# Performance work log

Hardware: AMD Instinct MI355X
Metric: run time of the kernel (lower is better)

## Reference

```python
import jax, jax.numpy as jnp
import numpy as np

N = 8192      # num_nodes
B = 16        # batch
IN_DIM = 2    # input_dim
HID = 64      # hid_dim
K = 2         # diffusion_steps
DEG = 16
E = N * DEG
F = IN_DIM + HID            # concat(input, state) feature dim
NUM_MAT = 2 * K + 1         # dual random walk: 2 matrices * K steps + identity


def _spmm(vals, rows, cols, x):
    # sparse [N,N] @ dense [N,M]: y[rows[e]] += vals[e] * x[cols[e]]
    return jax.ops.segment_sum(vals[:, None] * x[cols], rows, num_segments=N)


def _diff_conv(x, W, b, edge_src, edge_dst, vals1, vals2):
    # x: [B, N, F] -> [B, N*out_dim]; Chebyshev-like diffusion recursion
    x0 = jnp.transpose(x, (1, 2, 0)).reshape(N, F * B)  # [N, F*B]
    xs = [x0]
    # matrix 1 = D_out^-1 A (edges src->dst), matrix 2 = D_in^-1 A^T (edges dst->src)
    for rows, cols, vals in ((edge_src, edge_dst, vals1), (edge_dst, edge_src, vals2)):
        x1 = _spmm(vals, rows, cols, x0)
        xs.append(x1)
        xp, xc = x0, x1
        for _ in range(2, K + 1):
            xn = 2.0 * _spmm(vals, rows, cols, xc) - xp
            xs.append(xn)
            xp, xc = xc, xn
    xstk = jnp.stack(xs, 0).reshape(NUM_MAT, N, F, B)
    xstk = jnp.transpose(xstk, (3, 1, 2, 0)).reshape(B * N, F * NUM_MAT)
    out = xstk @ W + b  # [B*N, out_dim]
    return out.reshape(B, -1)


def setup_inputs() -> dict:
    key = jax.random.key(0)
    k = jax.random.split(key, 8)
    inputs = jax.random.normal(k[0], (B, N * IN_DIM), jnp.float32)
    state = jax.random.normal(k[1], (B, N * HID), jnp.float32)
    edge_src = jax.random.randint(k[2], (E,), 0, N)
    edge_dst = jax.random.randint(k[3], (E,), 0, N)
    a = jax.random.uniform(k[4], (E,), jnp.float32) + 0.1  # positive edge weights
    dout = jax.ops.segment_sum(a, edge_src, num_segments=N)
    din = jax.ops.segment_sum(a, edge_dst, num_segments=N)
    vals1 = a / jnp.where(dout > 0, dout, 1.0)[edge_src]  # random-walk normalize A
    vals2 = a / jnp.where(din > 0, din, 1.0)[edge_dst]    # random-walk normalize A^T
    std_g = 1.414 * np.sqrt(2.0 / (F * NUM_MAT + 2 * HID)).astype(np.float32)
    std_c = 1.414 * np.sqrt(2.0 / (F * NUM_MAT + HID)).astype(np.float32)
    W_gate = jax.random.normal(k[5], (F * NUM_MAT, 2 * HID), jnp.float32) * std_g
    b_gate = jnp.zeros((2 * HID,), jnp.float32)
    W_cand = jax.random.normal(k[6], (F * NUM_MAT, HID), jnp.float32) * std_c
    b_cand = jnp.zeros((HID,), jnp.float32)
    return dict(inputs=inputs, state=state, edge_src=edge_src, edge_dst=edge_dst,
                vals1=vals1, vals2=vals2, W_gate=W_gate, b_gate=b_gate,
                W_cand=W_cand, b_cand=b_cand)


def reference(inputs, state, edge_src, edge_dst, vals1, vals2,
              W_gate, b_gate, W_cand, b_cand):
    i = inputs.reshape(B, N, IN_DIM)
    s = state.reshape(B, N, HID)
    x = jnp.concatenate([i, s], axis=2)  # [B, N, F]
    value = jax.nn.sigmoid(_diff_conv(x, W_gate, b_gate, edge_src, edge_dst, vals1, vals2))
    value = value.reshape(B, N, 2 * HID)
    r = value[..., :HID].reshape(B, N * HID)
    u = value[..., HID:].reshape(B, N * HID)
    rs = (r * state).reshape(B, N, HID)
    xc = jnp.concatenate([i, rs], axis=2)
    c = jnp.tanh(_diff_conv(xc, W_cand, b_cand, edge_src, edge_dst, vals1, vals2))
    new_state = u * state + (1.0 - u) * c
    return (new_state, new_state)
```

## Files before the change

kernel.cpp:

```cpp
#include <hip/hip_runtime.h>
#include <cstddef>
#include <cstdint>

#define NNODES 8192
#define BATCH  16
#define HID    64
#define NEDGE  131072
#define SN     524288
#define OUTHALF 8388608
#define FP2    72
#define SLABU  1152
#define NSTR   5760
#define NSTR4  720
#define XCS4   144
#define KP2    384
#define GN     4

typedef __attribute__((ext_vector_type(8))) short bf16x8;
typedef __attribute__((ext_vector_type(4))) float f32x4;

static __device__ __forceinline__ float bf2f(ushort u) {
    union { uint32_t i; float f; } c; c.i = ((uint32_t)u) << 16; return c.f;
}
static __device__ __forceinline__ ushort f2bf(float f) {
    union { float f; uint32_t i; } c; c.f = f;
    uint32_t lsb = (c.i >> 16) & 1;
    return (ushort)((c.i + 0x7fffu + lsb) >> 16);
}


__global__ void zero_counts_kernel(int* __restrict__ c1, int* __restrict__ c2) {
    int i = blockIdx.x * 256 + threadIdx.x;
    if (i < NNODES) { c1[i] = 0; c2[i] = 0; }
}

__global__ void hist_kernel(const int* __restrict__ src, const int* __restrict__ dst,
                            int* __restrict__ c1, int* __restrict__ c2) {
    int e = blockIdx.x * 256 + threadIdx.x;
    if (e < NEDGE) {
        atomicAdd(&c1[src[e]], 1);
        atomicAdd(&c2[dst[e]], 1);
    }
}

__global__ __launch_bounds__(1024) void scan_kernel(const int* __restrict__ counts,
                                                    int* __restrict__ rowptr,
                                                    int* __restrict__ cursor) {
    __shared__ int sh[1024];
    int tid = threadIdx.x;
    int base = tid * 8;
    int local[8];
    int sum = 0;
#pragma unroll
    for (int j = 0; j < 8; ++j) { local[j] = counts[base + j]; sum += local[j]; }
    sh[tid] = sum;
    __syncthreads();
    for (int off = 1; off < 1024; off <<= 1) {
        int v = (tid >= off) ? sh[tid - off] : 0;
        __syncthreads();
        sh[tid] += v;
        __syncthreads();
    }
    int p = sh[tid] - sum;
#pragma unroll
    for (int j = 0; j < 8; ++j) {
        cursor[base + j] = p;
        p += local[j];
        rowptr[base + j + 1] = p;
    }
    if (tid == 0) rowptr[0] = 0;
}

__global__ void scatter_kernel(const int* __restrict__ src, const int* __restrict__ dst,
                               const float* __restrict__ v1, const float* __restrict__ v2,
                               int* __restrict__ cur1, int* __restrict__ cur2,
                               int* __restrict__ cols1, float* __restrict__ valsC1,
                               int* __restrict__ cols2, float* __restrict__ valsC2) {
    int e = blockIdx.x * 256 + threadIdx.x;
    if (e < NEDGE) {
        int r1 = src[e];
        int p1 = atomicAdd(&cur1[r1], 1);
        cols1[p1] = dst[e];
        valsC1[p1] = v1[e];
        int r2 = dst[e];
        int p2 = atomicAdd(&cur2[r2], 1);
        cols2[p2] = src[e];
        valsC2[p2] = v2[e];
    }
}


__global__ void convert_w_kernel(const float* __restrict__ Wg, const float* __restrict__ Wc,
                                 ushort* __restrict__ WgT, ushort* __restrict__ WcT) {
    int i = blockIdx.x * 256 + threadIdx.x;
    if (i >= 192 * KP2) return;
    int col = i / KP2, k2 = i - col * KP2;
    int m = k2 / FP2, f = k2 - m * FP2;
    bool valid = (m < 5) && (f < 66);
    int ko = f * 5 + m;
    if (col < 128) {
        WgT[col * KP2 + k2] = valid ? f2bf(Wg[ko * 128 + col]) : (ushort)0;
    } else {
        int c = col - 128;
        WcT[c * KP2 + k2] = valid ? f2bf(Wc[ko * 64 + c]) : (ushort)0;
    }
}


__global__ void build_x0_kernel(const float* __restrict__ inputs, const float* __restrict__ state,
                                uint* __restrict__ Xb_u, uint* __restrict__ Xc_u) {
    int t = blockIdx.x * 256 + threadIdx.x;
    if (t >= NNODES * BATCH * 36) return;
    int n = t / 576;
    int r = t - n * 576;
    int b = r / 36;
    int j = r - b * 36;
    int f0 = 2 * j;
    uint val = 0;
    if (f0 == 0) {
        float v0 = inputs[(size_t)b * (NNODES * 2) + n * 2 + 0];
        float v1 = inputs[(size_t)b * (NNODES * 2) + n * 2 + 1];
        val = (uint)f2bf(v0) | ((uint)f2bf(v1) << 16);
    } else if (f0 < 66) {
        float v0 = state[(size_t)b * SN + n * HID + (f0 - 2)];
        float v1 = state[(size_t)b * SN + n * HID + (f0 - 1)];
        val = (uint)f2bf(v0) | ((uint)f2bf(v1) << 16);
    }
    Xb_u[(size_t)n * 2880 + r] = val;
    if (f0 == 0 || f0 >= 66) Xc_u[t] = val;
}


static __device__ __forceinline__ void fma8(float* acc, uint4 d, float v) {
    acc[0] += v * bf2f((ushort)(d.x));  acc[1] += v * bf2f((ushort)(d.x >> 16));
    acc[2] += v * bf2f((ushort)(d.y));  acc[3] += v * bf2f((ushort)(d.y >> 16));
    acc[4] += v * bf2f((ushort)(d.z));  acc[5] += v * bf2f((ushort)(d.z >> 16));
    acc[6] += v * bf2f((ushort)(d.w));  acc[7] += v * bf2f((ushort)(d.w >> 16));
}

static __device__ __forceinline__ uint4 blend_pack8(const float* acc, uint4 p,
                                                    float alpha, float beta) {
    float o[8];
    o[0] = alpha * acc[0] + beta * bf2f((ushort)(p.x));
    o[1] = alpha * acc[1] + beta * bf2f((ushort)(p.x >> 16));
    o[2] = alpha * acc[2] + beta * bf2f((ushort)(p.y));
    o[3] = alpha * acc[3] + beta * bf2f((ushort)(p.y >> 16));
    o[4] = alpha * acc[4] + beta * bf2f((ushort)(p.z));
    o[5] = alpha * acc[5] + beta * bf2f((ushort)(p.z >> 16));
    o[6] = alpha * acc[6] + beta * bf2f((ushort)(p.w));
    o[7] = alpha * acc[7] + beta * bf2f((ushort)(p.w >> 16));
    uint4 r;
    r.x = (uint32_t)f2bf(o[0]) | ((uint32_t)f2bf(o[1]) << 16);
    r.y = (uint32_t)f2bf(o[2]) | ((uint32_t)f2bf(o[3]) << 16);
    r.z = (uint32_t)f2bf(o[4]) | ((uint32_t)f2bf(o[5]) << 16);
    r.w = (uint32_t)f2bf(o[6]) | ((uint32_t)f2bf(o[7]) << 16);
    return r;
}

__global__ __launch_bounds__(64) void spmm_dual8(
        const int* __restrict__ rp1, const int* __restrict__ c1, const float* __restrict__ v1,
        const uint4* __restrict__ x1,
        const int* __restrict__ rp2, const int* __restrict__ c2, const float* __restrict__ v2,
        const uint4* __restrict__ x2,
        int xs,
        const uint4* __restrict__ xp, int ps,
        uint4* __restrict__ y1, uint4* __restrict__ y2, int ys,
        float alpha, float beta) {
    int bid = blockIdx.x;
    int slice = bid & 7;
    int pair  = bid >> 3;
    int n     = pair & 8191;
    int graph = pair >> 13;
    const int* rowptr = graph ? rp2 : rp1;
    const int* cols   = graph ? c2 : c1;
    const float* vals = graph ? v2 : v1;
    const uint4* x    = graph ? x2 : x1;
    uint4* y          = graph ? y2 : y1;

    int t = threadIdx.x;
    int eg = t / 18;
    int li = t - eg * 18;
    int base = slice * 18 + li;
    bool active = t < 54;
    int s = rowptr[n], e = rowptr[n + 1];
    float acc[8] = {0, 0, 0, 0, 0, 0, 0, 0};
    const uint4 uz = make_uint4(0, 0, 0, 0);
    for (int i = s; i < e; i += 6) {
        int iA = i + eg, iB = i + 3 + eg;
        bool okA = active && (iA < e);
        bool okB = active && (iB < e);
        int cA  = okA ? cols[iA] : 0;
        int cB  = okB ? cols[iB] : 0;
        float vA = okA ? vals[iA] : 0.f;
        float vB = okB ? vals[iB] : 0.f;
        uint4 dA = okA ? x[(size_t)cA * xs + base] : uz;
        uint4 dB = okB ? x[(size_t)cB * xs + base] : uz;
        fma8(acc, dA, vA);
        fma8(acc, dB, vB);
    }
#pragma unroll
    for (int j = 0; j < 8; ++j) {
        float a18 = __shfl(acc[j], t + 18);
        float a36 = __shfl(acc[j], t + 36);
        acc[j] += a18 + a36;
    }
    if (t < 18) {
        uint4 p = (beta != 0.f) ? xp[(size_t)n * ps + base] : uz;
        y[(size_t)n * ys + base] = blend_pack8(acc, p, alpha, beta);
    }
}


__global__ __launch_bounds__(256, 2) void gate_mfma(const ushort* __restrict__ Xb,
                                                    const ushort* __restrict__ WgT,
                                                    const float* __restrict__ bg,
                                                    const float* __restrict__ state,
                                                    float* __restrict__ U,
                                                    ushort* __restrict__ Xc) {
    int tid = threadIdx.x;
    int wave = tid >> 6, lane = tid & 63;
    int row = lane & 15, quad = lane >> 4;
    int c0 = wave * 32 + row;
    int c1 = c0 + 16;

    bf16x8 w0[12], w1[12];
#pragma unroll
    for (int kt = 0; kt < 12; ++kt) {
        w0[kt] = *(const bf16x8*)(WgT + (size_t)c0 * KP2 + kt * 32 + quad * 8);
        w1[kt] = *(const bf16x8*)(WgT + (size_t)c1 * KP2 + kt * 32 + quad * 8);
    }
    float bias0 = bg[c0], bias1 = bg[c1];

    int offA[11];
#pragma unroll
    for (int kt = 0; kt < 11; ++kt) {
        int j = 4 * kt + quad;
        int m = j / 9;
        int f0 = 8 * (j - 9 * m);
        offA[kt] = m * SLABU + row * FP2 + f0;
    }
    int off11 = 4 * SLABU + row * FP2 + 64;

    int nodeBase = blockIdx.x * GN;
    for (int g = 0; g < GN; ++g) {
        int n = nodeBase + g;
        const ushort* An = Xb + (size_t)n * NSTR;
        f32x4 acc0 = {0.f, 0.f, 0.f, 0.f};
        f32x4 acc1 = {0.f, 0.f, 0.f, 0.f};
#pragma unroll
        for (int kt = 0; kt < 11; ++kt) {
            bf16x8 av = *(const bf16x8*)(An + offA[kt]);
            acc0 = __builtin_amdgcn_mfma_f32_16x16x32_bf16(av, w0[kt], acc0, 0, 0, 0);
            acc1 = __builtin_amdgcn_mfma_f32_16x16x32_bf16(av, w1[kt], acc1, 0, 0, 0);
        }
        {
            bf16x8 av = {0, 0, 0, 0, 0, 0, 0, 0};
            if (quad == 0) av = *(const bf16x8*)(An + off11);
            acc0 = __builtin_amdgcn_mfma_f32_16x16x32_bf16(av, w0[11], acc0, 0, 0, 0);
            acc1 = __builtin_amdgcn_mfma_f32_16x16x32_bf16(av, w1[11], acc1, 0, 0, 0);
        }
#pragma unroll
        for (int r = 0; r < 4; ++r) {
            int b = quad * 4 + r;
            float v0 = 1.f / (1.f + __expf(-(acc0[r] + bias0)));
            float v1 = 1.f / (1.f + __expf(-(acc1[r] + bias1)));
            if (wave < 2) {
                float s0 = state[(size_t)b * SN + n * HID + c0];
                float s1 = state[(size_t)b * SN + n * HID + c1];
                Xc[(size_t)n * SLABU + b * FP2 + 2 + c0] = f2bf(v0 * s0);
                Xc[(size_t)n * SLABU + b * FP2 + 2 + c1] = f2bf(v1 * s1);
            } else {
                U[(size_t)b * SN + n * HID + (c0 - HID)] = v0;
                U[(size_t)b * SN + n * HID + (c1 - HID)] = v1;
            }
        }
    }
}


__global__ __launch_bounds__(256, 2) void cand_mfma(const ushort* __restrict__ Xb,
                                                    const ushort* __restrict__ Xc,
                                                    const ushort* __restrict__ WcT,
                                                    const float* __restrict__ bc,
                                                    const float* __restrict__ state,
                                                    const float* U,
                                                    float* out) {
    int tid = threadIdx.x;
    int wave = tid >> 6, lane = tid & 63;
    int row = lane & 15, quad = lane >> 4;
    int c = wave * 16 + row;

    bf16x8 w[12];
#pragma unroll
    for (int kt = 0; kt < 12; ++kt)
        w[kt] = *(const bf16x8*)(WcT + (size_t)c * KP2 + kt * 32 + quad * 8);
    float bias = bc[c];

    int offA[11];
#pragma unroll
    for (int kt = 0; kt < 11; ++kt) {
        int j = 4 * kt + quad;
        int m = j / 9;
        int f0 = 8 * (j - 9 * m);
        offA[kt] = m * SLABU + row * FP2 + f0;
    }
    int off11 = 4 * SLABU + row * FP2 + 64;

    int nodeBase = blockIdx.x * GN;
    for (int g = 0; g < GN; ++g) {
        int n = nodeBase + g;
        const ushort* AnB = Xb + (size_t)n * NSTR;
        const ushort* AnC = Xc + (size_t)n * SLABU;
        f32x4 acc = {0.f, 0.f, 0.f, 0.f};
#pragma unroll
        for (int kt = 0; kt < 11; ++kt) {
            const ushort* bp = (kt < 2) ? AnC
                             : (kt == 2 ? (quad == 0 ? AnC : AnB) : AnB);
            bf16x8 av = *(const bf16x8*)(bp + offA[kt]);
            acc = __builtin_amdgcn_mfma_f32_16x16x32_bf16(av, w[kt], acc, 0, 0, 0);
        }
        {
            bf16x8 av = {0, 0, 0, 0, 0, 0, 0, 0};
            if (quad == 0) av = *(const bf16x8*)(AnB + off11);
            acc = __builtin_amdgcn_mfma_f32_16x16x32_bf16(av, w[11], acc, 0, 0, 0);
        }
#pragma unroll
        for (int r = 0; r < 4; ++r) {
            int b = quad * 4 + r;
            float pre = acc[r] + bias;
            float cv = 1.f - 2.f / (__expf(2.f * pre) + 1.f);
            size_t idx = (size_t)b * SN + n * HID + c;
            float uv = U[idx];
            float s = state[idx];
            float ns = uv * s + (1.f - uv) * cv;
            out[idx] = ns;
            out[OUTHALF + idx] = ns;
        }
    }
}


extern "C" void kernel_launch(void* const* d_in, const int* in_sizes, int n_in,
                              void* d_out, int out_size, void* d_ws, size_t ws_size,
                              hipStream_t stream) {
    const float* inputs = (const float*)d_in[0];
    const float* state  = (const float*)d_in[1];
    const int*   esrc   = (const int*)d_in[2];
    const int*   edst   = (const int*)d_in[3];
    const float* v1     = (const float*)d_in[4];
    const float* v2     = (const float*)d_in[5];
    const float* Wg     = (const float*)d_in[6];
    const float* bg     = (const float*)d_in[7];
    const float* Wc     = (const float*)d_in[8];
    const float* bc     = (const float*)d_in[9];
    float* out = (float*)d_out;

    char* ws = (char*)d_ws;
    size_t off = 0;
    auto alloc = [&](size_t bytes) -> void* {
        void* p = ws + off;
        off += (bytes + 255) & ~(size_t)255;
        return p;
    };
    ushort* Xb     = (ushort*)alloc((size_t)NNODES * NSTR * 2);
    ushort* Xc     = (ushort*)alloc((size_t)NNODES * SLABU * 2);
    ushort* WgT    = (ushort*)alloc((size_t)128 * KP2 * 2);
    ushort* WcT    = (ushort*)alloc((size_t)64 * KP2 * 2);
    int*   counts1 = (int*)alloc(NNODES * 4);
    int*   counts2 = (int*)alloc(NNODES * 4);
    int*   rowptr1 = (int*)alloc((NNODES + 1) * 4);
    int*   rowptr2 = (int*)alloc((NNODES + 1) * 4);
    int*   cursor1 = (int*)alloc(NNODES * 4);
    int*   cursor2 = (int*)alloc(NNODES * 4);
    int*   cols1   = (int*)alloc(NEDGE * 4);
    int*   cols2   = (int*)alloc(NEDGE * 4);
    float* valsC1  = (float*)alloc(NEDGE * 4);
    float* valsC2  = (float*)alloc(NEDGE * 4);

    float* U = out + OUTHALF;

    uint4* Xb4 = (uint4*)Xb;
    uint4* Xc4 = (uint4*)Xc;
    auto slab = [&](int m) { return Xb4 + (size_t)m * 144; };

    zero_counts_kernel<<<(NNODES + 255) / 256, 256, 0, stream>>>(counts1, counts2);
    hist_kernel<<<(NEDGE + 255) / 256, 256, 0, stream>>>(esrc, edst, counts1, counts2);
    scan_kernel<<<1, 1024, 0, stream>>>(counts1, rowptr1, cursor1);
    scan_kernel<<<1, 1024, 0, stream>>>(counts2, rowptr2, cursor2);
    scatter_kernel<<<(NEDGE + 255) / 256, 256, 0, stream>>>(esrc, edst, v1, v2,
                                                            cursor1, cursor2,
                                                            cols1, valsC1, cols2, valsC2);

    convert_w_kernel<<<(192 * KP2 + 255) / 256, 256, 0, stream>>>(Wg, Wc, WgT, WcT);
    build_x0_kernel<<<(NNODES * BATCH * 36 + 255) / 256, 256, 0, stream>>>(
        inputs, state, (uint*)Xb, (uint*)Xc);

    const int SPG = 2 * NNODES * 8;

    spmm_dual8<<<SPG, 64, 0, stream>>>(rowptr1, cols1, valsC1, slab(0),
                                       rowptr2, cols2, valsC2, slab(0), NSTR4,
                                       slab(0), NSTR4, slab(1), slab(3), NSTR4,
                                       1.f, 0.f);
    spmm_dual8<<<SPG, 64, 0, stream>>>(rowptr1, cols1, valsC1, slab(1),
                                       rowptr2, cols2, valsC2, slab(3), NSTR4,
                                       slab(0), NSTR4, slab(2), slab(4), NSTR4,
                                       2.f, -1.f);

    gate_mfma<<<NNODES / GN, 256, 0, stream>>>(Xb, WgT, bg, state, U, Xc);

    spmm_dual8<<<SPG, 64, 0, stream>>>(rowptr1, cols1, valsC1, Xc4,
                                       rowptr2, cols2, valsC2, Xc4, XCS4,
                                       Xc4, XCS4, slab(1), slab(3), NSTR4,
                                       1.f, 0.f);
    spmm_dual8<<<SPG, 64, 0, stream>>>(rowptr1, cols1, valsC1, slab(1),
                                       rowptr2, cols2, valsC2, slab(3), NSTR4,
                                       Xc4, XCS4, slab(2), slab(4), NSTR4,
                                       2.f, -1.f);

    cand_mfma<<<NNODES / GN, 256, 0, stream>>>(Xb, Xc, WcT, bc, state, U, out);
}
```

Measured before the change: 629.0 us.

## Reorganize feature slabs into batch-pair-sliced layout for SpMM locality

Changes the bf16 diffusion-feature buffers from node-major interleaved slabs to a layout sliced by batch pair, so each of the eight SpMM slices reads a contiguous 288-byte chunk per node from its own compact region. The goal is to shrink the working set each slice's gathers touch, improving L2/cache reuse of neighbor rows during random-column gathers. The MFMA gate and candidate kernels are updated to the new addressing, which now spreads each node's A-operand rows across distant slices and may weaken their load coalescing.

```diff
diff --git a/kernel.cpp b/kernel.cpp
--- a/kernel.cpp
+++ b/kernel.cpp
@@ -9,12 +9,14 @@
 #define SN     524288
 #define OUTHALF 8388608
 #define FP2    72
-#define SLABU  1152
-#define NSTR   5760
-#define NSTR4  720
-#define XCS4   144
 #define KP2    384
 #define GN     4
+
+#define CHUS   144
+#define CHU4   18
+#define SLAB_SL 1179648
+#define SLABT  9437184
+#define SLAB4  1179648
 
 typedef __attribute__((ext_vector_type(8))) short bf16x8;
 typedef __attribute__((ext_vector_type(4))) float f32x4;
@@ -126,8 +128,9 @@
         float v1 = state[(size_t)b * SN + n * HID + (f0 - 1)];
         val = (uint)f2bf(v0) | ((uint)f2bf(v1) << 16);
     }
-    Xb_u[(size_t)n * 2880 + r] = val;
-    if (f0 == 0 || f0 >= 66) Xc_u[t] = val;
+    size_t idx = ((size_t)(b >> 1) * NNODES + n) * 72 + (b & 1) * 36 + j;
+    Xb_u[idx] = val;
+    if (f0 == 0 || f0 >= 66) Xc_u[idx] = val;
 }
 
 
@@ -162,9 +165,8 @@
         const uint4* __restrict__ x1,
         const int* __restrict__ rp2, const int* __restrict__ c2, const float* __restrict__ v2,
         const uint4* __restrict__ x2,
-        int xs,
-        const uint4* __restrict__ xp, int ps,
-        uint4* __restrict__ y1, uint4* __restrict__ y2, int ys,
+        const uint4* __restrict__ xp,
+        uint4* __restrict__ y1, uint4* __restrict__ y2,
         float alpha, float beta) {
     int bid = blockIdx.x;
     int slice = bid & 7;
@@ -180,8 +182,8 @@
     int t = threadIdx.x;
     int eg = t / 18;
     int li = t - eg * 18;
-    int base = slice * 18 + li;
     bool active = t < 54;
+    size_t sliceBase = (size_t)slice * NNODES * CHU4;
     int s = rowptr[n], e = rowptr[n + 1];
     float acc[8] = {0, 0, 0, 0, 0, 0, 0, 0};
     const uint4 uz = make_uint4(0, 0, 0, 0);
@@ -193,8 +195,8 @@
         int cB  = okB ? cols[iB] : 0;
         float vA = okA ? vals[iA] : 0.f;
         float vB = okB ? vals[iB] : 0.f;
-        uint4 dA = okA ? x[(size_t)cA * xs + base] : uz;
-        uint4 dB = okB ? x[(size_t)cB * xs + base] : uz;
+        uint4 dA = okA ? x[sliceBase + (size_t)cA * CHU4 + li] : uz;
+        uint4 dB = okB ? x[sliceBase + (size_t)cB * CHU4 + li] : uz;
         fma8(acc, dA, vA);
         fma8(acc, dB, vB);
     }
@@ -205,8 +207,9 @@
         acc[j] += a18 + a36;
     }
     if (t < 18) {
-        uint4 p = (beta != 0.f) ? xp[(size_t)n * ps + base] : uz;
-        y[(size_t)n * ys + base] = blend_pack8(acc, p, alpha, beta);
+        size_t chunk = sliceBase + (size_t)n * CHU4 + t;
+        uint4 p = (beta != 0.f) ? xp[chunk] : uz;
+        y[chunk] = blend_pack8(acc, p, alpha, beta);
     }
 }
 
@@ -231,20 +234,21 @@
     }
     float bias0 = bg[c0], bias1 = bg[c1];
 
+    int rowOff = (row >> 1) * SLAB_SL + (row & 1) * FP2;
     int offA[11];
 #pragma unroll
     for (int kt = 0; kt < 11; ++kt) {
         int j = 4 * kt + quad;
         int m = j / 9;
         int f0 = 8 * (j - 9 * m);
-        offA[kt] = m * SLABU + row * FP2 + f0;
-    }
-    int off11 = 4 * SLABU + row * FP2 + 64;
+        offA[kt] = m * SLABT + rowOff + f0;
+    }
+    int off11 = 4 * SLABT + rowOff + 64;
 
     int nodeBase = blockIdx.x * GN;
     for (int g = 0; g < GN; ++g) {
         int n = nodeBase + g;
-        const ushort* An = Xb + (size_t)n * NSTR;
+        const ushort* An = Xb + (size_t)n * CHUS;
         f32x4 acc0 = {0.f, 0.f, 0.f, 0.f};
         f32x4 acc1 = {0.f, 0.f, 0.f, 0.f};
 #pragma unroll
@@ -267,8 +271,9 @@
             if (wave < 2) {
                 float s0 = state[(size_t)b * SN + n * HID + c0];
                 float s1 = state[(size_t)b * SN + n * HID + c1];
-                Xc[(size_t)n * SLABU + b * FP2 + 2 + c0] = f2bf(v0 * s0);
-                Xc[(size_t)n * SLABU + b * FP2 + 2 + c1] = f2bf(v1 * s1);
+                size_t cb = ((size_t)(b >> 1) * NNODES + n) * CHUS + (b & 1) * FP2;
+                Xc[cb + 2 + c0] = f2bf(v0 * s0);
+                Xc[cb + 2 + c1] = f2bf(v1 * s1);
             } else {
                 U[(size_t)b * SN + n * HID + (c0 - HID)] = v0;
                 U[(size_t)b * SN + n * HID + (c1 - HID)] = v1;
@@ -296,21 +301,22 @@
         w[kt] = *(const bf16x8*)(WcT + (size_t)c * KP2 + kt * 32 + quad * 8);
     float bias = bc[c];
 
+    int rowOff = (row >> 1) * SLAB_SL + (row & 1) * FP2;
     int offA[11];
 #pragma unroll
     for (int kt = 0; kt < 11; ++kt) {
         int j = 4 * kt + quad;
         int m = j / 9;
         int f0 = 8 * (j - 9 * m);
-        offA[kt] = m * SLABU + row * FP2 + f0;
-    }
-    int off11 = 4 * SLABU + row * FP2 + 64;
+        offA[kt] = m * SLABT + rowOff + f0;
+    }
+    int off11 = 4 * SLABT + rowOff + 64;
 
     int nodeBase = blockIdx.x * GN;
     for (int g = 0; g < GN; ++g) {
         int n = nodeBase + g;
-        const ushort* AnB = Xb + (size_t)n * NSTR;
-        const ushort* AnC = Xc + (size_t)n * SLABU;
+        const ushort* AnB = Xb + (size_t)n * CHUS;
+        const ushort* AnC = Xc + (size_t)n * CHUS;
         f32x4 acc = {0.f, 0.f, 0.f, 0.f};
 #pragma unroll
         for (int kt = 0; kt < 11; ++kt) {
@@ -362,8 +368,8 @@
         off += (bytes + 255) & ~(size_t)255;
         return p;
     };
-    ushort* Xb     = (ushort*)alloc((size_t)NNODES * NSTR * 2);
-    ushort* Xc     = (ushort*)alloc((size_t)NNODES * SLABU * 2);
+    ushort* Xb     = (ushort*)alloc((size_t)5 * SLABT * 2);
+    ushort* Xc     = (ushort*)alloc((size_t)SLABT * 2);
     ushort* WgT    = (ushort*)alloc((size_t)128 * KP2 * 2);
     ushort* WcT    = (ushort*)alloc((size_t)64 * KP2 * 2);
     int*   counts1 = (int*)alloc(NNODES * 4);
@@ -381,7 +387,7 @@
 
     uint4* Xb4 = (uint4*)Xb;
     uint4* Xc4 = (uint4*)Xc;
-    auto slab = [&](int m) { return Xb4 + (size_t)m * 144; };
+    auto slab = [&](int m) { return Xb4 + (size_t)m * SLAB4; };
 
     zero_counts_kernel<<<(NNODES + 255) / 256, 256, 0, stream>>>(counts1, counts2);
     hist_kernel<<<(NEDGE + 255) / 256, 256, 0, stream>>>(esrc, edst, counts1, counts2);
@@ -398,24 +404,20 @@
     const int SPG = 2 * NNODES * 8;
 
     spmm_dual8<<<SPG, 64, 0, stream>>>(rowptr1, cols1, valsC1, slab(0),
-                                       rowptr2, cols2, valsC2, slab(0), NSTR4,
-                                       slab(0), NSTR4, slab(1), slab(3), NSTR4,
-                                       1.f, 0.f);
+                                       rowptr2, cols2, valsC2, slab(0),
+                                       slab(0), slab(1), slab(3), 1.f, 0.f);
     spmm_dual8<<<SPG, 64, 0, stream>>>(rowptr1, cols1, valsC1, slab(1),
-                                       rowptr2, cols2, valsC2, slab(3), NSTR4,
-                                       slab(0), NSTR4, slab(2), slab(4), NSTR4,
-                                       2.f, -1.f);
+                                       rowptr2, cols2, valsC2, slab(3),
+                                       slab(0), slab(2), slab(4), 2.f, -1.f);
 
     gate_mfma<<<NNODES / GN, 256, 0, stream>>>(Xb, WgT, bg, state, U, Xc);
 
     spmm_dual8<<<SPG, 64, 0, stream>>>(rowptr1, cols1, valsC1, Xc4,
-                                       rowptr2, cols2, valsC2, Xc4, XCS4,
-                                       Xc4, XCS4, slab(1), slab(3), NSTR4,
-                                       1.f, 0.f);
+                                       rowptr2, cols2, valsC2, Xc4,
+                                       Xc4, slab(1), slab(3), 1.f, 0.f);
     spmm_dual8<<<SPG, 64, 0, stream>>>(rowptr1, cols1, valsC1, slab(1),
-                                       rowptr2, cols2, valsC2, slab(3), NSTR4,
-                                       Xc4, XCS4, slab(2), slab(4), NSTR4,
-                                       2.f, -1.f);
+                                       rowptr2, cols2, valsC2, slab(3),
+                                       Xc4, slab(2), slab(4), 2.f, -1.f);
 
     cand_mfma<<<NNODES / GN, 256, 0, stream>>>(Xb, Xc, WcT, bc, state, U, out);
 }
```

After: 919.2 us. 46.1% more time.
